# Optimization experiments

Measured on AMD Instinct MI355X. Metric: run time of the kernel, lower is better.

Reference implementation:

```python
import jax, jax.numpy as jnp
import numpy as np

D_MODEL, D_STATE, D_CONV, EXPAND = 1024, 16, 4, 2
D_INNER = EXPAND * D_MODEL
EPS = 1e-6


def setup_inputs() -> dict:
    key = jax.random.key(0)
    ks = jax.random.split(key, 8)
    B, T = 2, 1024
    s = lambda fan_in: 1.0 / np.sqrt(fan_in)
    x = jax.random.normal(ks[0], (B, T, D_MODEL), dtype=jnp.float32)
    norm_w = jnp.ones((D_MODEL,), jnp.float32)
    in_proj_w = jax.random.normal(ks[1], (D_MODEL, 2 * D_INNER), jnp.float32) * s(D_MODEL)
    conv_w = jax.random.normal(ks[2], (D_INNER, 1, D_CONV), jnp.float32) * s(D_CONV)
    dt_w = jax.random.normal(ks[3], (D_INNER, D_INNER), jnp.float32) * s(D_INNER)
    dt_b = jnp.zeros((D_INNER,), jnp.float32)
    # A_log init: log(arange(1..d_state)) repeated over d_inner rows
    A_log = jnp.log(jnp.broadcast_to(jnp.arange(1, D_STATE + 1, dtype=jnp.float32), (D_INNER, D_STATE)))
    B_w = jax.random.normal(ks[4], (D_INNER, D_STATE), jnp.float32) * s(D_INNER)
    C_w = jax.random.normal(ks[5], (D_INNER, D_STATE), jnp.float32) * s(D_INNER)
    D_skip = jnp.ones((D_INNER,), jnp.float32)
    out_proj_w = jax.random.normal(ks[6], (D_INNER, D_MODEL), jnp.float32) * s(D_INNER)
    return {"x": x, "norm_w": norm_w, "in_proj_w": in_proj_w, "conv_w": conv_w,
            "dt_w": dt_w, "dt_b": dt_b, "A_log": A_log, "B_w": B_w, "C_w": C_w,
            "D_skip": D_skip, "out_proj_w": out_proj_w}


def _forward(x, norm_w, in_proj_w, conv_w, dt_w, dt_b, A_log, B_w, C_w, D_skip, out_proj_w):
    Bsz, T, _ = x.shape
    # RMSNorm
    xn = x * jax.lax.rsqrt(jnp.mean(x * x, axis=-1, keepdims=True) + EPS) * norm_w
    # in_proj + gated silu
    xg = xn @ in_proj_w                                  # [B,T,2*di]
    x_inner, gate = jnp.split(xg, 2, axis=-1)
    x_inner = x_inner * jax.nn.silu(gate)                # [B,T,di]
    # causal depthwise conv (torch pads both sides then takes first T == left-pad only)
    xc = jax.lax.conv_general_dilated(
        x_inner.transpose(0, 2, 1), conv_w, window_strides=(1,),
        padding=[(D_CONV - 1, 0)], feature_group_count=D_INNER,
        dimension_numbers=("NCH", "OIH", "NCH")).transpose(0, 2, 1)  # [B,T,di]
    dt = jax.nn.softplus(xc @ dt_w + dt_b)               # [B,T,di]
    A = -jnp.exp(A_log)                                  # [di,ds]
    Bm = xc @ B_w                                        # [B,T,ds]
    Cm = xc @ C_w                                        # [B,T,ds]
    A_bar = jnp.exp(dt[..., None] * A)                   # [B,T,di,ds]
    B_bar = dt[..., None] * Bm[:, :, None, :]            # [B,T,di,ds]

    def step(h, inp):
        a_t, b_t, xc_t, c_t = inp                        # [B,di,ds],[B,di,ds],[B,di],[B,ds]
        h = a_t * h + b_t * xc_t[..., None]
        y = jnp.einsum("bds,bs->bd", h, c_t) + D_skip * xc_t
        return h, y

    h0 = jnp.zeros((Bsz, D_INNER, D_STATE), x.dtype)
    xs = (A_bar.transpose(1, 0, 2, 3), B_bar.transpose(1, 0, 2, 3),
          xc.transpose(1, 0, 2), Cm.transpose(1, 0, 2))
    _, ys = jax.lax.scan(step, h0, xs)                   # ys: [T,B,di]
    out = ys.transpose(1, 0, 2) @ out_proj_w             # [B,T,d_model]
    return out


def reference(x, norm_w, in_proj_w, conv_w, dt_w, dt_b, A_log, B_w, C_w, D_skip, out_proj_w):
    return _forward(x, norm_w, in_proj_w, conv_w, dt_w, dt_b, A_log, B_w, C_w, D_skip, out_proj_w)
```

## Files before the change

kernel.cpp:

```cpp
#include <hip/hip_runtime.h>
#include <cmath>


#define SEQ    1024
#define BATCH  2
#define DMODEL 1024
#define DINNER 2048
#define DSTATE 16
#define NTOK   (BATCH * SEQ)
#define NCHUNK 32
#define CLEN   32
#define NEXT   2112

typedef __attribute__((ext_vector_type(8))) short short8;
typedef __attribute__((ext_vector_type(4))) float f32x4;

__device__ __forceinline__ unsigned short f2bf(float f) {
  unsigned int u = __float_as_uint(f);
  unsigned int r = (u + 0x7fffu + ((u >> 16) & 1u)) >> 16;
  return (unsigned short)r;
}
__device__ __forceinline__ float bf2f(unsigned short v) {
  return __uint_as_float((unsigned int)v << 16);
}
__device__ __forceinline__ float softplus_f(float x) {
  return (x > 20.f) ? x : log1pf(__expf(x));
}
__device__ __forceinline__ void gload_lds16(const void* g, void* l) {
  __builtin_amdgcn_global_load_lds(
      (const __attribute__((address_space(1))) unsigned int*)g,
      (__attribute__((address_space(3))) unsigned int*)l, 16, 0, 0);
}

template <int N>
__device__ __forceinline__ void wait_vmcnt() {
  if constexpr (N <= 0)      asm volatile("s_waitcnt vmcnt(0)" ::: "memory");
  else if constexpr (N == 1) asm volatile("s_waitcnt vmcnt(1)" ::: "memory");
  else if constexpr (N == 2) asm volatile("s_waitcnt vmcnt(2)" ::: "memory");
  else if constexpr (N == 3) asm volatile("s_waitcnt vmcnt(3)" ::: "memory");
  else if constexpr (N == 4) asm volatile("s_waitcnt vmcnt(4)" ::: "memory");
  else if constexpr (N == 5) asm volatile("s_waitcnt vmcnt(5)" ::: "memory");
  else if constexpr (N == 6) asm volatile("s_waitcnt vmcnt(6)" ::: "memory");
  else                       asm volatile("s_waitcnt vmcnt(8)" ::: "memory");
}

__device__ __forceinline__ size_t tiled_off(int row, int k, int kblks) {
  return ((size_t)(row >> 4) * kblks + (k >> 5)) * 512
       + ((size_t)((row & 15) + (((k >> 3) & 3) << 4)) << 3) + (k & 7);
}

__global__ __launch_bounds__(256) void init_aneg_k(const float* __restrict__ A_log,
                                                   float* __restrict__ Aneg) {
  int i = blockIdx.x * 256 + threadIdx.x;
  Aneg[i] = -__expf(A_log[i]);
}

__global__ void transpose_cvt_k(const float* __restrict__ W, unsigned short* __restrict__ Wt,
                                int K, int N) {
  __shared__ float tile[32][33];
  int k0 = blockIdx.y * 32, n0 = blockIdx.x * 32;
  int tx = threadIdx.x, ty = threadIdx.y;
  int kblks = K >> 5;
#pragma unroll
  for (int i = 0; i < 32; i += 8)
    tile[ty + i][tx] = W[(size_t)(k0 + ty + i) * N + n0 + tx];
  __syncthreads();
#pragma unroll
  for (int i = 0; i < 32; i += 8)
    Wt[tiled_off(n0 + ty + i, k0 + tx, kblks)] = f2bf(tile[tx][ty + i]);
}

__global__ void build_w2t_k(const float* __restrict__ dt_w, const float* __restrict__ B_w,
                            const float* __restrict__ C_w, unsigned short* __restrict__ Wt) {
  __shared__ float tile[32][33];
  int k0 = blockIdx.x * 32, n0 = blockIdx.y * 32;
  int tx = threadIdx.x, ty = threadIdx.y;
  if (n0 < DINNER) {
#pragma unroll
    for (int i = 0; i < 32; i += 8)
      tile[ty + i][tx] = dt_w[(size_t)(k0 + ty + i) * DINNER + n0 + tx];
    __syncthreads();
#pragma unroll
    for (int i = 0; i < 32; i += 8)
      Wt[tiled_off(n0 + ty + i, k0 + tx, 64)] = f2bf(tile[tx][ty + i]);
  } else {
#pragma unroll
    for (int i = 0; i < 32; i += 8) {
      int n = n0 + ty + i;
      float v = 0.f;
      if (n < DINNER + 16) v = B_w[(size_t)(k0 + tx) * DSTATE + (n - DINNER)];
      else if (n < DINNER + 32) v = C_w[(size_t)(k0 + tx) * DSTATE + (n - DINNER - 16)];
      Wt[tiled_off(n, k0 + tx, 64)] = f2bf(v);
    }
  }
}

__global__ __launch_bounds__(256) void rmsnorm_k(const float* __restrict__ x,
                                                 const float* __restrict__ w,
                                                 unsigned short* __restrict__ xnbf) {
  int row = blockIdx.x, tid = threadIdx.x;
  const float4 v = *(const float4*)(x + (size_t)row * DMODEL + tid * 4);
  float ss = v.x * v.x + v.y * v.y + v.z * v.z + v.w * v.w;
#pragma unroll
  for (int off = 32; off > 0; off >>= 1) ss += __shfl_down(ss, off);
  __shared__ float red[4];
  if ((tid & 63) == 0) red[tid >> 6] = ss;
  __syncthreads();
  float tot = red[0] + red[1] + red[2] + red[3];
  float scale = rsqrtf(tot * (1.0f / DMODEL) + 1e-6f);
  const float4 wv = *(const float4*)(w + tid * 4);
  ushort4 o;
  o.x = f2bf(v.x * scale * wv.x);
  o.y = f2bf(v.y * scale * wv.y);
  o.z = f2bf(v.z * scale * wv.z);
  o.w = f2bf(v.w * scale * wv.w);
  *(ushort4*)(xnbf + tiled_off(row, tid * 4, DMODEL / 32)) = o;
}

template <int BM, int BN, int WM, int WN, int MODE>
__global__ __launch_bounds__(WM * WN * 64) void gemm_bf16_t(
    const unsigned short* __restrict__ At, const unsigned short* __restrict__ Btt,
    void* __restrict__ Cv, int M, int N, int K, int ldc,
    const float* __restrict__ bias, float* __restrict__ Bm, float* __restrict__ Cm) {
  constexpr int NW = WM * WN;
  constexpr int WTM = BM / WM, WTN = BN / WN;
  constexpr int FM = WTM / 16, FN = WTN / 16;
  constexpr int ASUB = BM / 16, BSUB = BN / 16;
  constexpr int ALOAD = ASUB * 2, BLOAD = BSUB * 2;
  constexpr int LPW = (ALOAD + BLOAD) / NW;
  static_assert(ALOAD % NW == 0 && BLOAD % NW == 0, "uniform load split");
  __shared__ __align__(16) unsigned short Abuf[2][BM * 64];
  __shared__ __align__(16) unsigned short Bbuf[2][BN * 64];
  const int tid = threadIdx.x;
  const int wave = tid >> 6, lane = tid & 63;

  int lin = blockIdx.x + blockIdx.y * gridDim.x;
  int nwg = gridDim.x * gridDim.y;
  int swz = (lin & 7) * (nwg >> 3) + (lin >> 3);
  const int MT = gridDim.y;
  const int bm = (swz % MT) * BM, bn = (swz / MT) * BN;

  const int wm = wave / WN, wn = wave % WN;
  const int kblks = K >> 5;
  const unsigned short* Ag = At + ((size_t)(bm >> 4) * kblks) * 512 + (lane << 3);
  const unsigned short* Bg = Btt + ((size_t)(bn >> 4) * kblks) * 512 + (lane << 3);

  auto stage = [&](int buf, int t) {
#pragma unroll
    for (int i = wave; i < ALOAD; i += NW) {
      int s = i >> 1, kk = i & 1;
      gload_lds16(Ag + ((size_t)s * kblks + 2 * t + kk) * 512,
                  &Abuf[buf][(kk * ASUB + s) * 512]);
    }
#pragma unroll
    for (int i = wave; i < BLOAD; i += NW) {
      int s = i >> 1, kk = i & 1;
      gload_lds16(Bg + ((size_t)s * kblks + 2 * t + kk) * 512,
                  &Bbuf[buf][(kk * BSUB + s) * 512]);
    }
  };

  f32x4 acc[FM][FN] = {};
  const int nt = K / 64;
  stage(0, 0);
  stage(1, 1);
  for (int t = 0; t < nt; ++t) {
    const int cur = t & 1;
    if (t + 1 < nt) wait_vmcnt<LPW>();
    else            wait_vmcnt<0>();
    __builtin_amdgcn_s_barrier();
    short8 af[2][FM], bfr[2][FN];
#pragma unroll
    for (int kk = 0; kk < 2; ++kk) {
#pragma unroll
      for (int m = 0; m < FM; ++m)
        af[kk][m] = *(const short8*)&Abuf[cur][(kk * ASUB + wm * FM + m) * 512 + (lane << 3)];
#pragma unroll
      for (int n = 0; n < FN; ++n)
        bfr[kk][n] = *(const short8*)&Bbuf[cur][(kk * BSUB + wn * FN + n) * 512 + (lane << 3)];
    }
    asm volatile("s_waitcnt lgkmcnt(0)" ::: "memory");
    __builtin_amdgcn_sched_barrier(0);
    __builtin_amdgcn_s_barrier();
    if (t + 2 < nt) stage(cur, t + 2);
#pragma unroll
    for (int kk = 0; kk < 2; ++kk)
#pragma unroll
      for (int m = 0; m < FM; ++m)
#pragma unroll
        for (int n = 0; n < FN; ++n)
          acc[m][n] = __builtin_amdgcn_mfma_f32_16x16x32_bf16(af[kk][m], bfr[kk][n],
                                                              acc[m][n], 0, 0, 0);
  }

  const int rbase = bm + wm * WTM + (lane >> 4) * 4;
  const int cbase = bn + wn * WTN + (lane & 15);
#pragma unroll
  for (int m = 0; m < FM; ++m)
#pragma unroll
    for (int n = 0; n < FN; ++n) {
      int col = cbase + n * 16;
#pragma unroll
      for (int r = 0; r < 4; ++r) {
        int row = rbase + m * 16 + r;
        float v = acc[m][n][r];
        if (MODE == 0) {
          ((float*)Cv)[(size_t)row * ldc + col] = v;
        } else if (MODE == 1) {
          ((unsigned short*)Cv)[(size_t)row * ldc + col] = f2bf(v);
        } else {
          if (col < DINNER)
            ((float*)Cv)[(size_t)row * DINNER + col] = softplus_f(v + bias[col]);
          else if (col < DINNER + 16)
            Bm[(size_t)row * DSTATE + (col - DINNER)] = v;
          else if (col < DINNER + 32)
            Cm[(size_t)row * DSTATE + (col - DINNER - 16)] = v;
        }
      }
    }
}

__global__ __launch_bounds__(256) void siluconv_k(const unsigned short* __restrict__ xg,
                                                  const float* __restrict__ w,
                                                  unsigned short* __restrict__ xcbf) {
  int idx = blockIdx.x * 256 + threadIdx.x;
  int d4 = (idx & 511) << 2;
  int tc = (idx >> 9) & 127;
  int b = idx >> 16;
  float4 w0 = *(const float4*)(w + (d4 + 0) * 4);
  float4 w1 = *(const float4*)(w + (d4 + 1) * 4);
  float4 w2 = *(const float4*)(w + (d4 + 2) * 4);
  float4 w3 = *(const float4*)(w + (d4 + 3) * 4);
  const float wj0[4] = {w0.x, w0.y, w0.z, w0.w};
  const float wj1[4] = {w1.x, w1.y, w1.z, w1.w};
  const float wj2[4] = {w2.x, w2.y, w2.z, w2.w};
  const float wj3[4] = {w3.x, w3.y, w3.z, w3.w};
  const unsigned short* pa = xg + (size_t)b * SEQ * (2 * DINNER) + d4;
  const unsigned short* pg = pa + DINNER;
  int t0 = tc * 8;
  float4 sA = {0.f, 0.f, 0.f, 0.f}, sB = sA, sC = sA;
  auto gated = [&](int t) {
    ushort4 av = *(const ushort4*)(pa + (size_t)t * (2 * DINNER));
    ushort4 gv = *(const ushort4*)(pg + (size_t)t * (2 * DINNER));
    float4 r;
    float gx = bf2f(gv.x), gy = bf2f(gv.y), gz = bf2f(gv.z), gw = bf2f(gv.w);
    r.x = bf2f(av.x) * (gx / (1.f + __expf(-gx)));
    r.y = bf2f(av.y) * (gy / (1.f + __expf(-gy)));
    r.z = bf2f(av.z) * (gz / (1.f + __expf(-gz)));
    r.w = bf2f(av.w) * (gw / (1.f + __expf(-gw)));
    return r;
  };
  if (t0 > 0) {
    sA = gated(t0 - 3);
    sB = gated(t0 - 2);
    sC = gated(t0 - 1);
  }
#pragma unroll
  for (int j = 0; j < 8; ++j) {
    int t = t0 + j;
    float4 sD = gated(t);
    float4 o;
    o.x = sA.x * wj0[0] + sB.x * wj0[1] + sC.x * wj0[2] + sD.x * wj0[3];
    o.y = sA.y * wj1[0] + sB.y * wj1[1] + sC.y * wj1[2] + sD.y * wj1[3];
    o.z = sA.z * wj2[0] + sB.z * wj2[1] + sC.z * wj2[2] + sD.z * wj2[3];
    o.w = sA.w * wj3[0] + sB.w * wj3[1] + sC.w * wj3[2] + sD.w * wj3[3];
    ushort4 ob = {f2bf(o.x), f2bf(o.y), f2bf(o.z), f2bf(o.w)};
    *(ushort4*)(xcbf + tiled_off(b * SEQ + t, d4, 64)) = ob;
    sA = sB; sB = sC; sC = sD;
  }
}

__global__ __launch_bounds__(256) void scan_local_k(const float* __restrict__ dt,
                                                    const unsigned short* __restrict__ xcbf,
                                                    const float* __restrict__ Bm,
                                                    const float* __restrict__ A,
                                                    float* __restrict__ hfin,
                                                    float* __restrict__ P) {
  int d = blockIdx.x * 256 + threadIdx.x;
  int c = blockIdx.y, b = blockIdx.z;
  float a[DSTATE], h[DSTATE];
#pragma unroll
  for (int s = 0; s < DSTATE; ++s) { a[s] = A[(size_t)d * DSTATE + s]; h[s] = 0.f; }
  float sdt = 0.f;
  int t0 = c * CLEN;
  for (int t = t0; t < t0 + CLEN; ++t) {
    size_t ro = (size_t)(b * SEQ + t);
    float dtv = dt[ro * DINNER + d];
    float xv = bf2f(xcbf[tiled_off((int)ro, d, 64)]);
    sdt += dtv;
    float bx = dtv * xv;
    float4 q0 = *(const float4*)(Bm + ro * DSTATE + 0);
    float4 q1 = *(const float4*)(Bm + ro * DSTATE + 4);
    float4 q2 = *(const float4*)(Bm + ro * DSTATE + 8);
    float4 q3 = *(const float4*)(Bm + ro * DSTATE + 12);
    float bm[DSTATE] = {q0.x, q0.y, q0.z, q0.w, q1.x, q1.y, q1.z, q1.w,
                        q2.x, q2.y, q2.z, q2.w, q3.x, q3.y, q3.z, q3.w};
#pragma unroll
    for (int s = 0; s < DSTATE; ++s) {
      float av = __expf(a[s] * dtv);
      h[s] = fmaf(av, h[s], bx * bm[s]);
    }
  }
  size_t o = ((size_t)(b * NCHUNK + c) * DINNER + d) * DSTATE;
#pragma unroll
  for (int s = 0; s < DSTATE; ++s) {
    hfin[o + s] = h[s];
    P[o + s] = __expf(a[s] * sdt);
  }
}

__global__ __launch_bounds__(256) void scan_chunks_k(float* hp, const float* __restrict__ P) {
  int j = blockIdx.x * 256 + threadIdx.x;
  int b = j / (DINNER * DSTATE);
  int r = j % (DINNER * DSTATE);
  float H = 0.f;
  for (int c = 0; c < NCHUNK; ++c) {
    size_t o = ((size_t)(b * NCHUNK + c) * DINNER * DSTATE) + r;
    float hf = hp[o];
    float pv = P[o];
    hp[o] = H;
    H = fmaf(pv, H, hf);
  }
}

__global__ __launch_bounds__(256) void scan_final_k(const float* __restrict__ dt,
                                                    const unsigned short* __restrict__ xcbf,
                                                    const float* __restrict__ Bm,
                                                    const float* __restrict__ Cm,
                                                    const float* __restrict__ A,
                                                    const float* __restrict__ Hprev,
                                                    const float* __restrict__ Dskip,
                                                    unsigned short* __restrict__ ysbf) {
  int d = blockIdx.x * 256 + threadIdx.x;
  int c = blockIdx.y, b = blockIdx.z;
  float a[DSTATE], h[DSTATE];
  size_t ho = ((size_t)(b * NCHUNK + c) * DINNER + d) * DSTATE;
#pragma unroll
  for (int s = 0; s < DSTATE; ++s) {
    a[s] = A[(size_t)d * DSTATE + s];
    h[s] = Hprev[ho + s];
  }
  float Dv = Dskip[d];
  int t0 = c * CLEN;
  for (int t = t0; t < t0 + CLEN; ++t) {
    size_t ro = (size_t)(b * SEQ + t);
    float dtv = dt[ro * DINNER + d];
    float xv = bf2f(xcbf[tiled_off((int)ro, d, 64)]);
    float bx = dtv * xv;
    float4 q0 = *(const float4*)(Bm + ro * DSTATE + 0);
    float4 q1 = *(const float4*)(Bm + ro * DSTATE + 4);
    float4 q2 = *(const float4*)(Bm + ro * DSTATE + 8);
    float4 q3 = *(const float4*)(Bm + ro * DSTATE + 12);
    float bm[DSTATE] = {q0.x, q0.y, q0.z, q0.w, q1.x, q1.y, q1.z, q1.w,
                        q2.x, q2.y, q2.z, q2.w, q3.x, q3.y, q3.z, q3.w};
    float4 r0 = *(const float4*)(Cm + ro * DSTATE + 0);
    float4 r1 = *(const float4*)(Cm + ro * DSTATE + 4);
    float4 r2 = *(const float4*)(Cm + ro * DSTATE + 8);
    float4 r3 = *(const float4*)(Cm + ro * DSTATE + 12);
    float cm[DSTATE] = {r0.x, r0.y, r0.z, r0.w, r1.x, r1.y, r1.z, r1.w,
                        r2.x, r2.y, r2.z, r2.w, r3.x, r3.y, r3.z, r3.w};
    float y = Dv * xv;
#pragma unroll
    for (int s = 0; s < DSTATE; ++s) {
      float av = __expf(a[s] * dtv);
      h[s] = fmaf(av, h[s], bx * bm[s]);
      y = fmaf(h[s], cm[s], y);
    }
    ysbf[tiled_off((int)ro, d, 64)] = f2bf(y);
  }
}

extern "C" void kernel_launch(void* const* d_in, const int* in_sizes, int n_in,
                              void* d_out, int out_size, void* d_ws, size_t ws_size,
                              hipStream_t stream) {
  (void)in_sizes; (void)n_in; (void)out_size; (void)ws_size;
  const float* x       = (const float*)d_in[0];
  const float* norm_w  = (const float*)d_in[1];
  const float* in_proj = (const float*)d_in[2];
  const float* conv_w  = (const float*)d_in[3];
  const float* dt_w    = (const float*)d_in[4];
  const float* dt_b    = (const float*)d_in[5];
  const float* A_log   = (const float*)d_in[6];
  const float* B_w     = (const float*)d_in[7];
  const float* C_w     = (const float*)d_in[8];
  const float* D_skip  = (const float*)d_in[9];
  const float* out_w   = (const float*)d_in[10];
  float* out = (float*)d_out;
  float* ws = (float*)d_ws;

  float* Aneg = ws;
  float* Bm   = ws + 32768;
  float* Cm   = ws + 65536;
  float* b0   = ws + 98304;
  unsigned short* xg = (unsigned short*)b0;
  float* dtb  = b0;
  float* hfin = b0 + 4194304;
  float* Pbuf = b0 + 6291456;
  unsigned short* xc_bf = (unsigned short*)(b0 + 8388608);
  unsigned short* ys_bf = (unsigned short*)(b0 + 10485760);
  float* Rw   = b0 + 12582912;
  unsigned short* in_wT  = (unsigned short*)Rw;
  unsigned short* W2t    = (unsigned short*)Rw;
  unsigned short* out_wT = (unsigned short*)Rw;
  unsigned short* xn_bf  = (unsigned short*)(b0 + 14745600);

  init_aneg_k<<<dim3(DINNER * DSTATE / 256), dim3(256), 0, stream>>>(A_log, Aneg);
  transpose_cvt_k<<<dim3(2 * DINNER / 32, DMODEL / 32), dim3(32, 8), 0, stream>>>(
      in_proj, in_wT, DMODEL, 2 * DINNER);
  rmsnorm_k<<<dim3(NTOK), dim3(256), 0, stream>>>(x, norm_w, xn_bf);
  gemm_bf16_t<128, 128, 2, 4, 1><<<dim3(2 * DINNER / 128, NTOK / 128), dim3(512), 0, stream>>>(
      xn_bf, in_wT, xg, NTOK, 2 * DINNER, DMODEL, 2 * DINNER, nullptr, nullptr, nullptr);
  siluconv_k<<<dim3(NTOK * (DINNER / 4) / 8 / 256), dim3(256), 0, stream>>>(
      xg, conv_w, xc_bf);
  build_w2t_k<<<dim3(DINNER / 32, NEXT / 32), dim3(32, 8), 0, stream>>>(
      dt_w, B_w, C_w, W2t);
  gemm_bf16_t<128, 64, 4, 2, 2><<<dim3(NEXT / 64, NTOK / 128), dim3(512), 0, stream>>>(
      xc_bf, W2t, dtb, NTOK, NEXT, DINNER, DINNER, dt_b, Bm, Cm);
  scan_local_k<<<dim3(DINNER / 256, NCHUNK, BATCH), dim3(256), 0, stream>>>(
      dtb, xc_bf, Bm, Aneg, hfin, Pbuf);
  scan_chunks_k<<<dim3(BATCH * DINNER * DSTATE / 256), dim3(256), 0, stream>>>(
      hfin, Pbuf);
  scan_final_k<<<dim3(DINNER / 256, NCHUNK, BATCH), dim3(256), 0, stream>>>(
      dtb, xc_bf, Bm, Cm, Aneg, hfin, D_skip, ys_bf);
  transpose_cvt_k<<<dim3(DMODEL / 32, DINNER / 32), dim3(32, 8), 0, stream>>>(
      out_w, out_wT, DINNER, DMODEL);
  gemm_bf16_t<64, 32, 2, 2, 0><<<dim3(DMODEL / 32, NTOK / 64), dim3(256), 0, stream>>>(
      ys_bf, out_wT, out, NTOK, DMODEL, DINNER, DMODEL, nullptr, nullptr, nullptr);
}
```

Baseline: 174.3 us.

## Switch GEMM to 4-stage pipeline with 32-wide K steps and retune tiles

The GEMM mainloop now loads one 32-wide K block per step into a 4-deep LDS ring buffer, instead of two K blocks into a double buffer. This keeps three stages of global-to-LDS loads in flight, which should hide more memory latency at the same LDS footprint. The cost is twice as many barriers and waits per unit of K. Launch configs also change: the dt/B/C GEMM drops to 4 waves (2x2) and the out_proj GEMM uses 64x64 tiles instead of 64x32, trading grid size against per-block reuse.

Result: slower. 195.5 us (+12.2%).

```diff
diff --git a/kernel.cpp b/kernel.cpp
--- a/kernel.cpp
+++ b/kernel.cpp
@@ -126,11 +126,10 @@
   constexpr int WTM = BM / WM, WTN = BN / WN;
   constexpr int FM = WTM / 16, FN = WTN / 16;
   constexpr int ASUB = BM / 16, BSUB = BN / 16;
-  constexpr int ALOAD = ASUB * 2, BLOAD = BSUB * 2;
-  constexpr int LPW = (ALOAD + BLOAD) / NW;
-  static_assert(ALOAD % NW == 0 && BLOAD % NW == 0, "uniform load split");
-  __shared__ __align__(16) unsigned short Abuf[2][BM * 64];
-  __shared__ __align__(16) unsigned short Bbuf[2][BN * 64];
+  constexpr int LPW = (ASUB + BSUB) / NW;
+  static_assert(ASUB % NW == 0 && BSUB % NW == 0, "uniform load split");
+  __shared__ __align__(16) unsigned short Abuf[4][BM * 32];
+  __shared__ __align__(16) unsigned short Bbuf[4][BN * 32];
   const int tid = threadIdx.x;
   const int wave = tid >> 6, lane = tid & 63;
 
@@ -147,50 +146,41 @@
 
   auto stage = [&](int buf, int t) {
 #pragma unroll
-    for (int i = wave; i < ALOAD; i += NW) {
-      int s = i >> 1, kk = i & 1;
-      gload_lds16(Ag + ((size_t)s * kblks + 2 * t + kk) * 512,
-                  &Abuf[buf][(kk * ASUB + s) * 512]);
-    }
-#pragma unroll
-    for (int i = wave; i < BLOAD; i += NW) {
-      int s = i >> 1, kk = i & 1;
-      gload_lds16(Bg + ((size_t)s * kblks + 2 * t + kk) * 512,
-                  &Bbuf[buf][(kk * BSUB + s) * 512]);
-    }
+    for (int s = wave; s < ASUB; s += NW)
+      gload_lds16(Ag + ((size_t)s * kblks + t) * 512, &Abuf[buf][s * 512]);
+#pragma unroll
+    for (int s = wave; s < BSUB; s += NW)
+      gload_lds16(Bg + ((size_t)s * kblks + t) * 512, &Bbuf[buf][s * 512]);
   };
 
   f32x4 acc[FM][FN] = {};
-  const int nt = K / 64;
+  const int nt = K / 32;
   stage(0, 0);
   stage(1, 1);
+  stage(2, 2);
   for (int t = 0; t < nt; ++t) {
-    const int cur = t & 1;
-    if (t + 1 < nt) wait_vmcnt<LPW>();
-    else            wait_vmcnt<0>();
+    const int cur = t & 3;
+    const int rem = nt - 1 - t;
+    if (rem >= 2)      wait_vmcnt<2 * LPW>();
+    else if (rem == 1) wait_vmcnt<LPW>();
+    else               wait_vmcnt<0>();
     __builtin_amdgcn_s_barrier();
-    short8 af[2][FM], bfr[2][FN];
-#pragma unroll
-    for (int kk = 0; kk < 2; ++kk) {
-#pragma unroll
-      for (int m = 0; m < FM; ++m)
-        af[kk][m] = *(const short8*)&Abuf[cur][(kk * ASUB + wm * FM + m) * 512 + (lane << 3)];
-#pragma unroll
-      for (int n = 0; n < FN; ++n)
-        bfr[kk][n] = *(const short8*)&Bbuf[cur][(kk * BSUB + wn * FN + n) * 512 + (lane << 3)];
-    }
+    short8 af[FM], bfr[FN];
+#pragma unroll
+    for (int m = 0; m < FM; ++m)
+      af[m] = *(const short8*)&Abuf[cur][(wm * FM + m) * 512 + (lane << 3)];
+#pragma unroll
+    for (int n = 0; n < FN; ++n)
+      bfr[n] = *(const short8*)&Bbuf[cur][(wn * FN + n) * 512 + (lane << 3)];
     asm volatile("s_waitcnt lgkmcnt(0)" ::: "memory");
     __builtin_amdgcn_sched_barrier(0);
     __builtin_amdgcn_s_barrier();
-    if (t + 2 < nt) stage(cur, t + 2);
-#pragma unroll
-    for (int kk = 0; kk < 2; ++kk)
-#pragma unroll
-      for (int m = 0; m < FM; ++m)
-#pragma unroll
-        for (int n = 0; n < FN; ++n)
-          acc[m][n] = __builtin_amdgcn_mfma_f32_16x16x32_bf16(af[kk][m], bfr[kk][n],
-                                                              acc[m][n], 0, 0, 0);
+    if (t + 3 < nt) stage((t + 3) & 3, t + 3);
+#pragma unroll
+    for (int m = 0; m < FM; ++m)
+#pragma unroll
+      for (int n = 0; n < FN; ++n)
+        acc[m][n] = __builtin_amdgcn_mfma_f32_16x16x32_bf16(af[m], bfr[n], acc[m][n], 0, 0, 0);
   }
 
   const int rbase = bm + wm * WTM + (lane >> 4) * 4;
@@ -414,7 +404,7 @@
       xg, conv_w, xc_bf);
   build_w2t_k<<<dim3(DINNER / 32, NEXT / 32), dim3(32, 8), 0, stream>>>(
       dt_w, B_w, C_w, W2t);
-  gemm_bf16_t<128, 64, 4, 2, 2><<<dim3(NEXT / 64, NTOK / 128), dim3(512), 0, stream>>>(
+  gemm_bf16_t<128, 64, 2, 2, 2><<<dim3(NEXT / 64, NTOK / 128), dim3(256), 0, stream>>>(
       xc_bf, W2t, dtb, NTOK, NEXT, DINNER, DINNER, dt_b, Bm, Cm);
   scan_local_k<<<dim3(DINNER / 256, NCHUNK, BATCH), dim3(256), 0, stream>>>(
       dtb, xc_bf, Bm, Aneg, hfin, Pbuf);
@@ -424,6 +414,6 @@
       dtb, xc_bf, Bm, Cm, Aneg, hfin, D_skip, ys_bf);
   transpose_cvt_k<<<dim3(DMODEL / 32, DINNER / 32), dim3(32, 8), 0, stream>>>(
       out_w, out_wT, DINNER, DMODEL);
-  gemm_bf16_t<64, 32, 2, 2, 0><<<dim3(DMODEL / 32, NTOK / 64), dim3(256), 0, stream>>>(
+  gemm_bf16_t<64, 64, 2, 2, 0><<<dim3(DMODEL / 64, NTOK / 64), dim3(256), 0, stream>>>(
       ys_bf, out_wT, out, NTOK, DMODEL, DINNER, DMODEL, nullptr, nullptr, nullptr);
 }
```

## Triple-buffer LDS in bf16 GEMM and drop the second per-iteration barrier

Applied to the files above, without the earlier changes.

The GEMM kernel moves from two static LDS buffers to three in dynamic shared memory. The prefetch for tile t+2 is issued right after the top-of-loop barrier into the third buffer, so the lgkmcnt wait and the second barrier between fragment reads and the next stage are gone. The dt/B/C GEMM also changes from 4x2 waves (512 threads) to 2x2 waves (256 threads) with larger per-wave tiles. This costs more LDS per block, which may lower occupancy, and the new wave layout puts more accumulator registers on each wave.

Result: slower. 202.1 us (+16.0%).

```diff
diff --git a/kernel.cpp b/kernel.cpp
--- a/kernel.cpp
+++ b/kernel.cpp
@@ -41,7 +41,8 @@
   else if constexpr (N == 4) asm volatile("s_waitcnt vmcnt(4)" ::: "memory");
   else if constexpr (N == 5) asm volatile("s_waitcnt vmcnt(5)" ::: "memory");
   else if constexpr (N == 6) asm volatile("s_waitcnt vmcnt(6)" ::: "memory");
-  else                       asm volatile("s_waitcnt vmcnt(8)" ::: "memory");
+  else if constexpr (N == 8) asm volatile("s_waitcnt vmcnt(8)" ::: "memory");
+  else                       asm volatile("s_waitcnt vmcnt(12)" ::: "memory");
 }
 
 __device__ __forceinline__ size_t tiled_off(int row, int k, int kblks) {
@@ -118,7 +119,7 @@
 }
 
 template <int BM, int BN, int WM, int WN, int MODE>
-__global__ __launch_bounds__(WM * WN * 64) void gemm_bf16_t(
+__global__ __launch_bounds__(WM * WN * 64) void gemm3(
     const unsigned short* __restrict__ At, const unsigned short* __restrict__ Btt,
     void* __restrict__ Cv, int M, int N, int K, int ldc,
     const float* __restrict__ bias, float* __restrict__ Bm, float* __restrict__ Cm) {
@@ -128,9 +129,10 @@
   constexpr int ASUB = BM / 16, BSUB = BN / 16;
   constexpr int ALOAD = ASUB * 2, BLOAD = BSUB * 2;
   constexpr int LPW = (ALOAD + BLOAD) / NW;
+  constexpr int TBUF = (BM + BN) * 64;
+  constexpr int BOFF = BM * 64;
   static_assert(ALOAD % NW == 0 && BLOAD % NW == 0, "uniform load split");
-  __shared__ __align__(16) unsigned short Abuf[2][BM * 64];
-  __shared__ __align__(16) unsigned short Bbuf[2][BN * 64];
+  extern __shared__ __align__(16) unsigned short smem[];
   const int tid = threadIdx.x;
   const int wave = tid >> 6, lane = tid & 63;
 
@@ -150,13 +152,13 @@
     for (int i = wave; i < ALOAD; i += NW) {
       int s = i >> 1, kk = i & 1;
       gload_lds16(Ag + ((size_t)s * kblks + 2 * t + kk) * 512,
-                  &Abuf[buf][(kk * ASUB + s) * 512]);
+                  smem + buf * TBUF + (kk * ASUB + s) * 512);
     }
 #pragma unroll
     for (int i = wave; i < BLOAD; i += NW) {
       int s = i >> 1, kk = i & 1;
       gload_lds16(Bg + ((size_t)s * kblks + 2 * t + kk) * 512,
-                  &Bbuf[buf][(kk * BSUB + s) * 512]);
+                  smem + buf * TBUF + BOFF + (kk * BSUB + s) * 512);
     }
   };
 
@@ -164,25 +166,26 @@
   const int nt = K / 64;
   stage(0, 0);
   stage(1, 1);
+  int cur = 0;
   for (int t = 0; t < nt; ++t) {
-    const int cur = t & 1;
     if (t + 1 < nt) wait_vmcnt<LPW>();
     else            wait_vmcnt<0>();
     __builtin_amdgcn_s_barrier();
+    __builtin_amdgcn_sched_barrier(0);
+    int nxt = cur + 2; if (nxt >= 3) nxt -= 3;
+    if (t + 2 < nt) stage(nxt, t + 2);
+    const unsigned short* bufA = smem + cur * TBUF;
+    const unsigned short* bufB = bufA + BOFF;
     short8 af[2][FM], bfr[2][FN];
 #pragma unroll
     for (int kk = 0; kk < 2; ++kk) {
 #pragma unroll
       for (int m = 0; m < FM; ++m)
-        af[kk][m] = *(const short8*)&Abuf[cur][(kk * ASUB + wm * FM + m) * 512 + (lane << 3)];
+        af[kk][m] = *(const short8*)(bufA + (kk * ASUB + wm * FM + m) * 512 + (lane << 3));
 #pragma unroll
       for (int n = 0; n < FN; ++n)
-        bfr[kk][n] = *(const short8*)&Bbuf[cur][(kk * BSUB + wn * FN + n) * 512 + (lane << 3)];
-    }
-    asm volatile("s_waitcnt lgkmcnt(0)" ::: "memory");
-    __builtin_amdgcn_sched_barrier(0);
-    __builtin_amdgcn_s_barrier();
-    if (t + 2 < nt) stage(cur, t + 2);
+        bfr[kk][n] = *(const short8*)(bufB + (kk * BSUB + wn * FN + n) * 512 + (lane << 3));
+    }
 #pragma unroll
     for (int kk = 0; kk < 2; ++kk)
 #pragma unroll
@@ -191,6 +194,7 @@
         for (int n = 0; n < FN; ++n)
           acc[m][n] = __builtin_amdgcn_mfma_f32_16x16x32_bf16(af[kk][m], bfr[kk][n],
                                                               acc[m][n], 0, 0, 0);
+    cur = cur + 1; if (cur >= 3) cur = 0;
   }
 
   const int rbase = bm + wm * WTM + (lane >> 4) * 4;
@@ -404,17 +408,27 @@
   unsigned short* out_wT = (unsigned short*)Rw;
   unsigned short* xn_bf  = (unsigned short*)(b0 + 14745600);
 
+  constexpr int LDS_IN  = 3 * (128 + 128) * 64 * 2;
+  constexpr int LDS_DT  = 3 * (128 + 64) * 64 * 2;
+  constexpr int LDS_OUT = 3 * (64 + 32) * 64 * 2;
+  (void)hipFuncSetAttribute((const void*)&gemm3<128, 128, 2, 4, 1>,
+                            hipFuncAttributeMaxDynamicSharedMemorySize, LDS_IN);
+  (void)hipFuncSetAttribute((const void*)&gemm3<128, 64, 2, 2, 2>,
+                            hipFuncAttributeMaxDynamicSharedMemorySize, LDS_DT);
+  (void)hipFuncSetAttribute((const void*)&gemm3<64, 32, 2, 2, 0>,
+                            hipFuncAttributeMaxDynamicSharedMemorySize, LDS_OUT);
+
   init_aneg_k<<<dim3(DINNER * DSTATE / 256), dim3(256), 0, stream>>>(A_log, Aneg);
   transpose_cvt_k<<<dim3(2 * DINNER / 32, DMODEL / 32), dim3(32, 8), 0, stream>>>(
       in_proj, in_wT, DMODEL, 2 * DINNER);
   rmsnorm_k<<<dim3(NTOK), dim3(256), 0, stream>>>(x, norm_w, xn_bf);
-  gemm_bf16_t<128, 128, 2, 4, 1><<<dim3(2 * DINNER / 128, NTOK / 128), dim3(512), 0, stream>>>(
+  gemm3<128, 128, 2, 4, 1><<<dim3(2 * DINNER / 128, NTOK / 128), dim3(512), LDS_IN, stream>>>(
       xn_bf, in_wT, xg, NTOK, 2 * DINNER, DMODEL, 2 * DINNER, nullptr, nullptr, nullptr);
   siluconv_k<<<dim3(NTOK * (DINNER / 4) / 8 / 256), dim3(256), 0, stream>>>(
       xg, conv_w, xc_bf);
   build_w2t_k<<<dim3(DINNER / 32, NEXT / 32), dim3(32, 8), 0, stream>>>(
       dt_w, B_w, C_w, W2t);
-  gemm_bf16_t<128, 64, 4, 2, 2><<<dim3(NEXT / 64, NTOK / 128), dim3(512), 0, stream>>>(
+  gemm3<128, 64, 2, 2, 2><<<dim3(NEXT / 64, NTOK / 128), dim3(256), LDS_DT, stream>>>(
       xc_bf, W2t, dtb, NTOK, NEXT, DINNER, DINNER, dt_b, Bm, Cm);
   scan_local_k<<<dim3(DINNER / 256, NCHUNK, BATCH), dim3(256), 0, stream>>>(
       dtb, xc_bf, Bm, Aneg, hfin, Pbuf);
@@ -424,6 +438,6 @@
       dtb, xc_bf, Bm, Cm, Aneg, hfin, D_skip, ys_bf);
   transpose_cvt_k<<<dim3(DMODEL / 32, DINNER / 32), dim3(32, 8), 0, stream>>>(
       out_w, out_wT, DINNER, DMODEL);
-  gemm_bf16_t<64, 32, 2, 2, 0><<<dim3(DMODEL / 32, NTOK / 64), dim3(256), 0, stream>>>(
+  gemm3<64, 32, 2, 2, 0><<<dim3(DMODEL / 32, NTOK / 64), dim3(256), LDS_OUT, stream>>>(
       ys_bf, out_wT, out, NTOK, DMODEL, DINNER, DMODEL, nullptr, nullptr, nullptr);
 }
```

## Split-K out_proj GEMM with larger tiles and a separate reduction kernel

Applied to the files above, without the earlier changes.

The out_proj GEMM moves from 64x32 tiles with 4 waves to 128x64 tiles with 8 waves. K is split in two across blockIdx.z, each half writing fp32 partials into workspace, and a new elementwise kernel sums the halves into the output. The goal is to keep a reasonable grid size (512 blocks) while using larger tiles with better data reuse per block. The cost is an extra launch plus writing and reading 2x8MB of fp32 partials.

Result: no change. 174.8 us (+0.3%).

```diff
diff --git a/kernel.cpp b/kernel.cpp
--- a/kernel.cpp
+++ b/kernel.cpp
@@ -41,7 +41,8 @@
   else if constexpr (N == 4) asm volatile("s_waitcnt vmcnt(4)" ::: "memory");
   else if constexpr (N == 5) asm volatile("s_waitcnt vmcnt(5)" ::: "memory");
   else if constexpr (N == 6) asm volatile("s_waitcnt vmcnt(6)" ::: "memory");
-  else                       asm volatile("s_waitcnt vmcnt(8)" ::: "memory");
+  else if constexpr (N == 8) asm volatile("s_waitcnt vmcnt(8)" ::: "memory");
+  else                       asm volatile("s_waitcnt vmcnt(12)" ::: "memory");
 }
 
 __device__ __forceinline__ size_t tiled_off(int row, int k, int kblks) {
@@ -117,10 +118,10 @@
   *(ushort4*)(xnbf + tiled_off(row, tid * 4, DMODEL / 32)) = o;
 }
 
-template <int BM, int BN, int WM, int WN, int MODE>
+template <int BM, int BN, int WM, int WN, int MODE, int SPLITZ>
 __global__ __launch_bounds__(WM * WN * 64) void gemm_bf16_t(
     const unsigned short* __restrict__ At, const unsigned short* __restrict__ Btt,
-    void* __restrict__ Cv, int M, int N, int K, int ldc,
+    void* __restrict__ Cv, int M, int N, int K, int kstride, int ldc,
     const float* __restrict__ bias, float* __restrict__ Bm, float* __restrict__ Cm) {
   constexpr int NW = WM * WN;
   constexpr int WTM = BM / WM, WTN = BN / WN;
@@ -140,22 +141,25 @@
   const int MT = gridDim.y;
   const int bm = (swz % MT) * BM, bn = (swz / MT) * BN;
 
+  const int koff = SPLITZ ? blockIdx.z * (K >> 5) : 0;
+  float* Cf = (float*)Cv;
+  if (SPLITZ) Cf += (size_t)blockIdx.z * M * ldc;
+
   const int wm = wave / WN, wn = wave % WN;
-  const int kblks = K >> 5;
-  const unsigned short* Ag = At + ((size_t)(bm >> 4) * kblks) * 512 + (lane << 3);
-  const unsigned short* Bg = Btt + ((size_t)(bn >> 4) * kblks) * 512 + (lane << 3);
+  const unsigned short* Ag = At + ((size_t)(bm >> 4) * kstride + koff) * 512 + (lane << 3);
+  const unsigned short* Bg = Btt + ((size_t)(bn >> 4) * kstride + koff) * 512 + (lane << 3);
 
   auto stage = [&](int buf, int t) {
 #pragma unroll
     for (int i = wave; i < ALOAD; i += NW) {
       int s = i >> 1, kk = i & 1;
-      gload_lds16(Ag + ((size_t)s * kblks + 2 * t + kk) * 512,
+      gload_lds16(Ag + ((size_t)s * kstride + 2 * t + kk) * 512,
                   &Abuf[buf][(kk * ASUB + s) * 512]);
     }
 #pragma unroll
     for (int i = wave; i < BLOAD; i += NW) {
       int s = i >> 1, kk = i & 1;
-      gload_lds16(Bg + ((size_t)s * kblks + 2 * t + kk) * 512,
+      gload_lds16(Bg + ((size_t)s * kstride + 2 * t + kk) * 512,
                   &Bbuf[buf][(kk * BSUB + s) * 512]);
     }
   };
@@ -205,7 +209,7 @@
         int row = rbase + m * 16 + r;
         float v = acc[m][n][r];
         if (MODE == 0) {
-          ((float*)Cv)[(size_t)row * ldc + col] = v;
+          Cf[(size_t)row * ldc + col] = v;
         } else if (MODE == 1) {
           ((unsigned short*)Cv)[(size_t)row * ldc + col] = f2bf(v);
         } else {
@@ -218,6 +222,16 @@
         }
       }
     }
+}
+
+__global__ __launch_bounds__(256) void reduce2_k(const float* __restrict__ P0,
+                                                 const float* __restrict__ P1,
+                                                 float* __restrict__ out) {
+  int i = (blockIdx.x * 256 + threadIdx.x) * 4;
+  float4 a = *(const float4*)(P0 + i);
+  float4 b = *(const float4*)(P1 + i);
+  float4 o = {a.x + b.x, a.y + b.y, a.z + b.z, a.w + b.w};
+  *(float4*)(out + i) = o;
 }
 
 __global__ __launch_bounds__(256) void siluconv_k(const unsigned short* __restrict__ xg,
@@ -396,6 +410,7 @@
   float* dtb  = b0;
   float* hfin = b0 + 4194304;
   float* Pbuf = b0 + 6291456;
+  float* outP = b0;
   unsigned short* xc_bf = (unsigned short*)(b0 + 8388608);
   unsigned short* ys_bf = (unsigned short*)(b0 + 10485760);
   float* Rw   = b0 + 12582912;
@@ -408,14 +423,17 @@
   transpose_cvt_k<<<dim3(2 * DINNER / 32, DMODEL / 32), dim3(32, 8), 0, stream>>>(
       in_proj, in_wT, DMODEL, 2 * DINNER);
   rmsnorm_k<<<dim3(NTOK), dim3(256), 0, stream>>>(x, norm_w, xn_bf);
-  gemm_bf16_t<128, 128, 2, 4, 1><<<dim3(2 * DINNER / 128, NTOK / 128), dim3(512), 0, stream>>>(
-      xn_bf, in_wT, xg, NTOK, 2 * DINNER, DMODEL, 2 * DINNER, nullptr, nullptr, nullptr);
+  gemm_bf16_t<128, 128, 2, 4, 1, 0>
+      <<<dim3(2 * DINNER / 128, NTOK / 128), dim3(512), 0, stream>>>(
+      xn_bf, in_wT, xg, NTOK, 2 * DINNER, DMODEL, DMODEL / 32, 2 * DINNER,
+      nullptr, nullptr, nullptr);
   siluconv_k<<<dim3(NTOK * (DINNER / 4) / 8 / 256), dim3(256), 0, stream>>>(
       xg, conv_w, xc_bf);
   build_w2t_k<<<dim3(DINNER / 32, NEXT / 32), dim3(32, 8), 0, stream>>>(
       dt_w, B_w, C_w, W2t);
-  gemm_bf16_t<128, 64, 4, 2, 2><<<dim3(NEXT / 64, NTOK / 128), dim3(512), 0, stream>>>(
-      xc_bf, W2t, dtb, NTOK, NEXT, DINNER, DINNER, dt_b, Bm, Cm);
+  gemm_bf16_t<128, 64, 4, 2, 2, 0>
+      <<<dim3(NEXT / 64, NTOK / 128), dim3(512), 0, stream>>>(
+      xc_bf, W2t, dtb, NTOK, NEXT, DINNER, DINNER / 32, DINNER, dt_b, Bm, Cm);
   scan_local_k<<<dim3(DINNER / 256, NCHUNK, BATCH), dim3(256), 0, stream>>>(
       dtb, xc_bf, Bm, Aneg, hfin, Pbuf);
   scan_chunks_k<<<dim3(BATCH * DINNER * DSTATE / 256), dim3(256), 0, stream>>>(
@@ -424,6 +442,10 @@
       dtb, xc_bf, Bm, Cm, Aneg, hfin, D_skip, ys_bf);
   transpose_cvt_k<<<dim3(DMODEL / 32, DINNER / 32), dim3(32, 8), 0, stream>>>(
       out_w, out_wT, DINNER, DMODEL);
-  gemm_bf16_t<64, 32, 2, 2, 0><<<dim3(DMODEL / 32, NTOK / 64), dim3(256), 0, stream>>>(
-      ys_bf, out_wT, out, NTOK, DMODEL, DINNER, DMODEL, nullptr, nullptr, nullptr);
-}
+  gemm_bf16_t<128, 64, 4, 2, 0, 1>
+      <<<dim3(DMODEL / 64, NTOK / 128, 2), dim3(512), 0, stream>>>(
+      ys_bf, out_wT, outP, NTOK, DMODEL, DINNER / 2, DINNER / 32, DMODEL,
+      nullptr, nullptr, nullptr);
+  reduce2_k<<<dim3(NTOK * DMODEL / 4 / 256), dim3(256), 0, stream>>>(
+      outP, outP + (size_t)NTOK * DMODEL, out);
+}
```
